# Kernel tuning notes

Hardware: AMD Instinct MI355X
Metric: run time of the kernel (lower is better)

Reference implementation:

```python
import jax, jax.numpy as jnp
import numpy as np

B, N, C, H, AD, HID = 2, 1024, 768, 12, 8, 3072
SCALE = (C // H) ** -0.5


def setup_inputs() -> dict:
    key = jax.random.key(0)
    ks = jax.random.split(key, 32)
    inp = {}
    for i in range(5):
        inp[f"x{i}"] = jax.random.normal(ks[i], (B, N, C), jnp.float32)
    def w(i, shape, s=0.02):
        return jax.random.normal(ks[i], shape, jnp.float32) * s
    inp.update({
        "ln1_g": jnp.ones((C,), jnp.float32), "ln1_b": jnp.zeros((C,), jnp.float32),
        "ln2_g": jnp.ones((C,), jnp.float32), "ln2_b": jnp.zeros((C,), jnp.float32),
        "qkv_w": w(5, (C, 3 * C)), "qkv_b": jnp.zeros((3 * C,), jnp.float32),
        "proj_w": w(6, (C, C)), "proj_b": jnp.zeros((C,), jnp.float32),
        "fc1_w": w(7, (C, HID)), "fc1_b": jnp.zeros((HID,), jnp.float32),
        "fc2_w": w(8, (HID, C)), "fc2_b": jnp.zeros((C,), jnp.float32),
        "at_dw": w(9, (C, AD)), "at_db": jnp.zeros((AD,), jnp.float32),
        "at_mw": w(10, (AD, AD)), "at_mb": jnp.zeros((AD,), jnp.float32),
        "at_uw": w(11, (AD, C)), "at_ub": jnp.zeros((C,), jnp.float32),
        "a2_dw": w(12, (C, AD)), "a2_db": jnp.zeros((AD,), jnp.float32),
        "a2_mw": w(13, (AD, AD)), "a2_mb": jnp.zeros((AD,), jnp.float32),
        "a2_uw": w(14, (AD, C)), "a2_ub": jnp.zeros((C,), jnp.float32),
    })
    return inp


def _ln(x, g, b, eps=1e-5):
    mu = x.mean(-1, keepdims=True)
    xc = x - mu
    var = (xc * xc).mean(-1, keepdims=True)
    return xc * jax.lax.rsqrt(var + eps) * g + b


def _adapter(x, dw, db, mw, mb, uw, ub):
    h = x @ dw + db          # bottleneck down [., AD]
    h = h @ mw + mb          # mid
    return h @ uw + ub       # up back to C


def _attn(x, qkv_w, qkv_b, proj_w, proj_b):
    # x: [S, B, N, C] (streams folded in leading axis)
    s, b, n, c = x.shape
    qkv = (x @ qkv_w + qkv_b).reshape(s, b, n, 3, H, c // H)
    q, k, v = jnp.moveaxis(qkv, 3, 0)            # each [S,B,N,H,D]
    scores = jnp.einsum('sbnhd,sbmhd->sbhnm', q * SCALE, k)  # fp32; clamp is a no-op
    p = jax.nn.softmax(scores, axis=-1)
    o = jnp.einsum('sbhnm,sbmhd->sbnhd', p, v).reshape(s, b, n, c)
    return o @ proj_w + proj_b


def reference(x0, x1, x2, x3, x4,
              ln1_g, ln1_b, ln2_g, ln2_b,
              qkv_w, qkv_b, proj_w, proj_b,
              fc1_w, fc1_b, fc2_w, fc2_b,
              at_dw, at_db, at_mw, at_mb, at_uw, at_ub,
              a2_dw, a2_db, a2_mw, a2_mb, a2_uw, a2_ub):
    xs = jnp.stack([x0, x1, x2, x3, x4])          # [5,B,N,C]
    n1 = _ln(xs, ln1_g, ln1_b)
    a1 = _adapter(n1, at_dw, at_db, at_mw, at_mb, at_uw, at_ub)
    ao = _attn(n1, qkv_w, qkv_b, proj_w, proj_b)
    # cross-stream residuals: x01=a1[0], x12=a1[1], ..., x10=a1[1], x21=a1[2], ...
    y0 = xs[0] + ao[0] + a1[1]
    y1 = xs[1] + ao[1] + a1[0] + a1[2]
    y2 = xs[2] + ao[2] + a1[1] + a1[3]
    y3 = xs[3] + ao[3] + a1[2] + a1[4]
    y4 = xs[4] + ao[4] + a1[3]
    ys = jnp.stack([y0, y1, y2, y3, y4])
    a2 = _adapter(_ln(ys, ln1_g, ln1_b), a2_dw, a2_db, a2_mw, a2_mb, a2_uw, a2_ub)
    h = _ln(ys, ln2_g, ln2_b) @ fc1_w + fc1_b
    m = jax.nn.gelu(h, approximate=False) @ fc2_w + fc2_b
    z0 = ys[0] + m[0] + a2[1]
    z1 = ys[1] + m[1] + a2[0] + a2[2]
    z2 = ys[2] + m[2] + a2[1] + a2[3]
    z3 = ys[3] + m[3] + a2[2] + a2[4]
    z4 = ys[4] + m[4] + a2[3]
    return jnp.stack([z0, z1, z2, z3, z4])        # [5,B,N,C]
```

## Files before the change

kernel.cpp:

```cpp
#include <hip/hip_runtime.h>
#include <math.h>

typedef __bf16 bf16;
typedef __attribute__((ext_vector_type(8))) __bf16 bf16x8;
typedef __attribute__((ext_vector_type(4))) __bf16 bf16x4;
typedef __attribute__((ext_vector_type(4))) float f32x4;
typedef __attribute__((ext_vector_type(16))) float f32x16;

#define TOK   10240
#define CD    768
#define NQKV  2304
#define NHID  3072
#define SEQ   1024
#define NH    12

__device__ __forceinline__ f32x4 mfma16(bf16x8 a, bf16x8 b, f32x4 c) {
  return __builtin_amdgcn_mfma_f32_16x16x32_bf16(a, b, c, 0, 0, 0);
}
__device__ __forceinline__ f32x16 mfma32(bf16x8 a, bf16x8 b, f32x16 c) {
  return __builtin_amdgcn_mfma_f32_32x32x16_bf16(a, b, c, 0, 0, 0);
}

__device__ __forceinline__ void gload16(const void* g, void* l) {
  __builtin_amdgcn_global_load_lds(
      (const __attribute__((address_space(1))) void*)g,
      (__attribute__((address_space(3))) void*)l, 16, 0, 0);
}

__device__ __forceinline__ unsigned pack2(bf16 a, bf16 b) {
  union { unsigned short u[2]; unsigned v; } x;
  x.u[0] = __builtin_bit_cast(unsigned short, a);
  x.u[1] = __builtin_bit_cast(unsigned short, b);
  return x.v;
}

__device__ __forceinline__ float fast_gelu(float v) {
  float u = 0.7978845608f * (v + 0.044715f * v * v * v);
  float e = __expf(fminf(2.f * u, 30.f));
  return 0.5f * v * (1.f + (e - 1.f) / (e + 1.f));
}

__global__ __launch_bounds__(256) void transpose_to_bf16(
    const float* __restrict__ in, bf16* __restrict__ out, int K, int N) {
  __shared__ float tile[32][33];
  const int bn = blockIdx.x * 32, bk = blockIdx.y * 32;
  const int r = threadIdx.x >> 5, c = threadIdx.x & 31;
#pragma unroll
  for (int i = 0; i < 4; ++i)
    tile[r + 8 * i][c] = in[(size_t)(bk + r + 8 * i) * N + bn + c];
  __syncthreads();
#pragma unroll
  for (int i = 0; i < 4; ++i)
    out[(size_t)(bn + r + 8 * i) * K + bk + c] = (bf16)tile[c][r + 8 * i];
}

__global__ __launch_bounds__(256) void ln5_kernel(
    const float* __restrict__ x0, const float* __restrict__ x1,
    const float* __restrict__ x2, const float* __restrict__ x3,
    const float* __restrict__ x4, const float* __restrict__ g,
    const float* __restrict__ b, bf16* __restrict__ out) {
  const int w = threadIdx.x >> 6, lane = threadIdx.x & 63;
  const int row = blockIdx.x * 4 + w;
  const int s = row >> 11, rem = row & 2047;
  const float* xp;
  switch (s) {
    case 0: xp = x0; break; case 1: xp = x1; break; case 2: xp = x2; break;
    case 3: xp = x3; break; default: xp = x4; break;
  }
  const f32x4* xr = (const f32x4*)(xp + (size_t)rem * CD);
  f32x4 v[3];
#pragma unroll
  for (int i = 0; i < 3; ++i) v[i] = xr[lane + 64 * i];
  float sum = 0.f;
#pragma unroll
  for (int i = 0; i < 3; ++i)
#pragma unroll
    for (int j = 0; j < 4; ++j) sum += v[i][j];
#pragma unroll
  for (int m = 32; m >= 1; m >>= 1) sum += __shfl_xor(sum, m);
  const float mu = sum * (1.f / 768.f);
  float vs = 0.f;
#pragma unroll
  for (int i = 0; i < 3; ++i)
#pragma unroll
    for (int j = 0; j < 4; ++j) { float d = v[i][j] - mu; vs += d * d; }
#pragma unroll
  for (int m = 32; m >= 1; m >>= 1) vs += __shfl_xor(vs, m);
  const float rstd = rsqrtf(vs * (1.f / 768.f) + 1e-5f);
  const f32x4* gp = (const f32x4*)g;
  const f32x4* bp = (const f32x4*)b;
  bf16* orow = out + (size_t)row * CD;
#pragma unroll
  for (int i = 0; i < 3; ++i) {
    const int c4 = lane + 64 * i;
    f32x4 gg = gp[c4], bb = bp[c4];
    bf16x4 o;
#pragma unroll
    for (int j = 0; j < 4; ++j)
      o[j] = (bf16)((v[i][j] - mu) * rstd * gg[j] + bb[j]);
    *(bf16x4*)(orow + c4 * 4) = o;
  }
}

__global__ __launch_bounds__(256) void fuse_res_ln(
    const float* __restrict__ x0, const float* __restrict__ x1,
    const float* __restrict__ x2, const float* __restrict__ x3,
    const float* __restrict__ x4, const float* __restrict__ add,
    const float* __restrict__ a, float* __restrict__ ys,
    const float* __restrict__ g1, const float* __restrict__ b1,
    const float* __restrict__ g2, const float* __restrict__ b2,
    bf16* __restrict__ o1, bf16* __restrict__ o2) {
  const int w = threadIdx.x >> 6, lane = threadIdx.x & 63;
  const int row = blockIdx.x * 4 + w;
  const int s = row >> 11, rem = row & 2047;
  const float* xp;
  switch (s) {
    case 0: xp = x0; break; case 1: xp = x1; break; case 2: xp = x2; break;
    case 3: xp = x3; break; default: xp = x4; break;
  }
  const f32x4* xr = (const f32x4*)(xp + (size_t)rem * CD);
  const f32x4* ar = (const f32x4*)(add + (size_t)row * CD);
  const f32x4* am = (const f32x4*)(a + (size_t)(row - 2048) * CD);
  const f32x4* ap = (const f32x4*)(a + (size_t)(row + 2048) * CD);
  f32x4 v[3];
#pragma unroll
  for (int i = 0; i < 3; ++i) {
    const int c4 = lane + 64 * i;
    f32x4 t = xr[c4] + ar[c4];
    if (s > 0) t += am[c4];
    if (s < 4) t += ap[c4];
    v[i] = t;
  }
  f32x4* yr = (f32x4*)(ys + (size_t)row * CD);
#pragma unroll
  for (int i = 0; i < 3; ++i) yr[lane + 64 * i] = v[i];

  float sum = 0.f;
#pragma unroll
  for (int i = 0; i < 3; ++i)
#pragma unroll
    for (int j = 0; j < 4; ++j) sum += v[i][j];
#pragma unroll
  for (int m = 32; m >= 1; m >>= 1) sum += __shfl_xor(sum, m);
  const float mu = sum * (1.f / 768.f);
  float vs = 0.f;
#pragma unroll
  for (int i = 0; i < 3; ++i)
#pragma unroll
    for (int j = 0; j < 4; ++j) { float d = v[i][j] - mu; vs += d * d; }
#pragma unroll
  for (int m = 32; m >= 1; m >>= 1) vs += __shfl_xor(vs, m);
  const float rstd = rsqrtf(vs * (1.f / 768.f) + 1e-5f);
  bf16* r1 = o1 + (size_t)row * CD;
  bf16* r2 = o2 + (size_t)row * CD;
#pragma unroll
  for (int i = 0; i < 3; ++i) {
    const int c4 = lane + 64 * i;
    f32x4 gg1 = ((const f32x4*)g1)[c4], bb1 = ((const f32x4*)b1)[c4];
    f32x4 gg2 = ((const f32x4*)g2)[c4], bb2 = ((const f32x4*)b2)[c4];
    bf16x4 oa, ob;
#pragma unroll
    for (int j = 0; j < 4; ++j) {
      float n = (v[i][j] - mu) * rstd;
      oa[j] = (bf16)(n * gg1[j] + bb1[j]);
      ob[j] = (bf16)(n * gg2[j] + bb2[j]);
    }
    *(bf16x4*)(r1 + c4 * 4) = oa;
    *(bf16x4*)(r2 + c4 * 4) = ob;
  }
}

#define GBAR() __builtin_amdgcn_s_barrier()

#define LOADA(MH, BUF)                                                      \
  _Pragma("unroll") for (int m_ = 0; m_ < 4; ++m_) {                        \
    af[m_][0] =                                                             \
        *(const bf16x8*)&As[BUF][((MH)*128 + arow + m_ * 16) * 64 + ach0];  \
    af[m_][1] =                                                             \
        *(const bf16x8*)&As[BUF][((MH)*128 + arow + m_ * 16) * 64 + ach1];  \
  }

#define LOADB(DST, NH, BUF)                                                 \
  _Pragma("unroll") for (int n_ = 0; n_ < 2; ++n_) {                        \
    DST[n_][0] =                                                            \
        *(const bf16x8*)&Bs[BUF][(brow + (NH)*32 + n_ * 16) * 64 + ach0];   \
    DST[n_][1] =                                                            \
        *(const bf16x8*)&Bs[BUF][(brow + (NH)*32 + n_ * 16) * 64 + ach1];   \
  }

#define MFMA_PH(MH, NH, BF)                                                 \
  __builtin_amdgcn_s_setprio(1);                                            \
  _Pragma("unroll") for (int m_ = 0; m_ < 4; ++m_)                          \
  _Pragma("unroll") for (int n_ = 0; n_ < 2; ++n_) {                        \
    acc[(MH)*4 + m_][(NH)*2 + n_] =                                         \
        mfma16(af[m_][0], BF[n_][0], acc[(MH)*4 + m_][(NH)*2 + n_]);        \
    acc[(MH)*4 + m_][(NH)*2 + n_] =                                         \
        mfma16(af[m_][1], BF[n_][1], acc[(MH)*4 + m_][(NH)*2 + n_]);        \
  }                                                                         \
  __builtin_amdgcn_s_setprio(0);

template <int EPI>
__global__ __launch_bounds__(512, 2) void gemm256(
    const bf16* __restrict__ A, const bf16* __restrict__ Bt,
    const float* __restrict__ bias, void* __restrict__ Cout, int N, int K,
    int nbn) {
  __shared__ bf16 As[2][16384];
  __shared__ bf16 Bs[2][16384];
  const int t = threadIdx.x, lane = t & 63, w = t >> 6;
  const int wm = w >> 2, wn = w & 3;

  const int chunkg = gridDim.x >> 3;
  const int wg = (blockIdx.x & 7) * chunkg + (blockIdx.x >> 3);
  const int bm = wg / nbn, bn = wg % nbn;

  f32x4 acc[8][4] = {};

  const int srow = t >> 3;
  const int scol = ((t & 7) ^ (srow & 7)) << 3;
  const bf16* Ab = A + (size_t)(bm * 256 + srow) * K + scol;
  const bf16* Bb = Bt + (size_t)(bn * 256 + srow) * K + scol;
  const size_t r64 = (size_t)64 * K;

  auto stage_a = [&](int buf, int h, int kt) {
    const bf16* g = Ab + (size_t)h * 128 * K + (size_t)kt * 64;
    gload16(g, &As[buf][h * 8192 + w * 512]);
    gload16(g + r64, &As[buf][h * 8192 + 4096 + w * 512]);
  };
  auto stage_b = [&](int buf, int h, int kt) {
    const bf16* g = Bb + (size_t)h * 128 * K + (size_t)kt * 64;
    gload16(g, &Bs[buf][h * 8192 + w * 512]);
    gload16(g + r64, &Bs[buf][h * 8192 + 4096 + w * 512]);
  };

  const int arow = wm * 64 + (lane & 15);
  const int brow = wn * 64 + (lane & 15);
  const int ach0 = (((lane >> 4) + 0) ^ (lane & 7)) << 3;
  const int ach1 = (((lane >> 4) + 4) ^ (lane & 7)) << 3;

  stage_a(0, 0, 0); stage_b(0, 0, 0); stage_b(0, 1, 0); stage_a(0, 1, 0);
  stage_a(1, 0, 1); stage_b(1, 0, 1);
  asm volatile("s_waitcnt vmcnt(4)" ::: "memory");
  GBAR();

  const int NT = K >> 6, NI = NT >> 1;
  bf16x8 af[4][2], bf0[2][2], bf1[2][2];

  for (int j = 0; j < NI; ++j) {
    const int tA = 2 * j, tB = 2 * j + 1;
    const bool notlast = (j + 1 < NI);

    LOADA(0, 0);
    LOADB(bf0, 0, 0);
    stage_b(1, 1, tB);
    GBAR();
    MFMA_PH(0, 0, bf0);
    GBAR();
    LOADB(bf1, 1, 0);
    stage_a(1, 1, tB);
    GBAR();
    MFMA_PH(0, 1, bf1);
    GBAR();
    LOADA(1, 0);
    if (notlast) stage_a(0, 0, tA + 2);
    GBAR();
    MFMA_PH(1, 0, bf0);
    GBAR();
    if (notlast) {
      stage_b(0, 0, tA + 2);
      asm volatile("s_waitcnt vmcnt(4)" ::: "memory");
    } else {
      asm volatile("s_waitcnt vmcnt(0)" ::: "memory");
    }
    GBAR();
    MFMA_PH(1, 1, bf1);
    GBAR();

    LOADA(0, 1);
    LOADB(bf0, 0, 1);
    if (notlast) stage_b(0, 1, tA + 2);
    GBAR();
    MFMA_PH(0, 0, bf0);
    GBAR();
    LOADB(bf1, 1, 1);
    if (notlast) stage_a(0, 1, tA + 2);
    GBAR();
    MFMA_PH(0, 1, bf1);
    GBAR();
    LOADA(1, 1);
    if (notlast) stage_a(1, 0, tB + 2);
    GBAR();
    MFMA_PH(1, 0, bf0);
    GBAR();
    if (notlast) {
      stage_b(1, 0, tB + 2);
      asm volatile("s_waitcnt vmcnt(4)" ::: "memory");
    }
    GBAR();
    MFMA_PH(1, 1, bf1);
    GBAR();
  }

#pragma unroll
  for (int am = 0; am < 8; ++am) {
    const int grow0 =
        bm * 256 + (am >> 2) * 128 + wm * 64 + (am & 3) * 16 + (lane >> 4) * 4;
#pragma unroll
    for (int an = 0; an < 4; ++an) {
      const int gcol = bn * 256 + wn * 64 + an * 16 + (lane & 15);
      const float bv = bias[gcol];
#pragma unroll
      for (int r = 0; r < 4; ++r) {
        float v = acc[am][an][r] + bv;
        if (EPI == 2) v = fast_gelu(v);
        const size_t idx = (size_t)(grow0 + r) * N + gcol;
        if (EPI == 0) ((float*)Cout)[idx] = v;
        else ((bf16*)Cout)[idx] = (bf16)v;
      }
    }
  }
}

__global__ __launch_bounds__(256, 3) void attn_v2(
    const bf16* __restrict__ qkv, bf16* __restrict__ obuf) {
  __shared__ bf16 Ks[2][4096];
  __shared__ bf16 Vt[2][4096];
  const int t = threadIdx.x, lane = t & 63, w = t >> 6;
  const int g = lane >> 5, q32 = lane & 31, rq7 = q32 & 7;

  const int xcd = blockIdx.x & 7, slot = blockIdx.x >> 3;
  const int work = xcd * 120 + slot;
  const int sbh = work >> 3, qt = work & 7;
  const int sb = sbh / NH, h = sbh % NH;
  const size_t tokbase = (size_t)sb * SEQ;
  const int qoff = h * 64, koff = CD + h * 64, voff = 2 * CD + h * 64;

  const int qrow = qt * 128 + w * 32 + q32;
  bf16x8 qf[4];
  {
    const bf16* qp = qkv + (tokbase + qrow) * NQKV + qoff + g * 8;
#pragma unroll
    for (int kd = 0; kd < 4; ++kd) {
      bf16x8 v = *(const bf16x8*)(qp + kd * 16);
#pragma unroll
      for (int j = 0; j < 8; ++j) v[j] = (bf16)((float)v[j] * 0.125f);
      qf[kd] = v;
    }
  }

  const int skv1 = t >> 3, sc1 = (t & 7) ^ (skv1 & 7);
  const int skv2 = (t + 256) >> 3, sc2 = (t & 7) ^ (skv2 & 7);
  const int vkv0 = 2 * (t & 31);
  const int vd0 = 8 * (t >> 5);
  const int c0 = (vkv0 & 51) | ((vkv0 & 4) << 1) | ((vkv0 & 8) >> 1);
  const int vchunk = c0 >> 3, vsub = c0 & 7;
  const bf16* kbase = qkv + tokbase * NQKV + koff;
  const bf16* vbase = qkv + tokbase * NQKV + voff;

  {
    const bf16* kb0 = kbase;
    gload16(kb0 + (size_t)skv1 * NQKV + sc1 * 8, &Ks[0][w * 512]);
    gload16(kb0 + (size_t)skv2 * NQKV + sc2 * 8, &Ks[0][2048 + w * 512]);
    const bf16* vp = vbase + (size_t)vkv0 * NQKV + vd0;
    bf16x8 r0 = *(const bf16x8*)vp;
    bf16x8 r1 = *(const bf16x8*)(vp + NQKV);
#pragma unroll
    for (int j = 0; j < 8; ++j) {
      const int d = vd0 + j;
      *(unsigned*)&Vt[0][d * 64 + ((vchunk ^ j) << 3) + vsub] =
          pack2(r0[j], r1[j]);
    }
  }
  __syncthreads();

  float m_run = -1e30f, l_run = 0.f;
  f32x16 oT0 = {}, oT1 = {};
  int cur = 0;

  for (int kt = 0; kt < 16; ++kt) {
    bf16x8 nv0, nv1;
    if (kt < 15) {
      const bf16* vp = vbase + (size_t)((kt + 1) * 64 + vkv0) * NQKV + vd0;
      nv0 = *(const bf16x8*)vp;
      nv1 = *(const bf16x8*)(vp + NQKV);
      const bf16* kb0 = kbase + (size_t)(kt + 1) * 64 * NQKV;
      gload16(kb0 + (size_t)skv1 * NQKV + sc1 * 8, &Ks[cur ^ 1][w * 512]);
      gload16(kb0 + (size_t)skv2 * NQKV + sc2 * 8,
              &Ks[cur ^ 1][2048 + w * 512]);
    }

    f32x16 sT0 = {}, sT1 = {};
#pragma unroll
    for (int kd = 0; kd < 4; ++kd) {
      bf16x8 kf0 =
          *(const bf16x8*)&Ks[cur][q32 * 64 + (((2 * kd + g) ^ rq7) << 3)];
      bf16x8 kf1 = *(const bf16x8*)&Ks[cur][(32 + q32) * 64 +
                                            (((2 * kd + g) ^ rq7) << 3)];
      sT0 = mfma32(kf0, qf[kd], sT0);
      sT1 = mfma32(kf1, qf[kd], sT1);
    }

    float mt = sT0[0];
#pragma unroll
    for (int r = 1; r < 16; ++r) mt = fmaxf(mt, sT0[r]);
#pragma unroll
    for (int r = 0; r < 16; ++r) mt = fmaxf(mt, sT1[r]);
    mt = fmaxf(mt, __shfl_xor(mt, 32));
    const float mnew = fmaxf(m_run, mt);
    const float alpha = __expf(m_run - mnew);
    m_run = mnew;
    float rs = 0.f;
#pragma unroll
    for (int r = 0; r < 16; ++r) {
      sT0[r] = __expf(sT0[r] - mnew);
      rs += sT0[r];
    }
#pragma unroll
    for (int r = 0; r < 16; ++r) {
      sT1[r] = __expf(sT1[r] - mnew);
      rs += sT1[r];
    }
    rs += __shfl_xor(rs, 32);
    l_run = l_run * alpha + rs;
#pragma unroll
    for (int r = 0; r < 16; ++r) { oT0[r] *= alpha; oT1[r] *= alpha; }

    bf16x8 pa[4];
#pragma unroll
    for (int hh = 0; hh < 2; ++hh)
#pragma unroll
      for (int j = 0; j < 8; ++j) {
        pa[hh][j] = (bf16)sT0[8 * hh + j];
        pa[2 + hh][j] = (bf16)sT1[8 * hh + j];
      }

#pragma unroll
    for (int ks = 0; ks < 4; ++ks) {
      bf16x8 vf0 =
          *(const bf16x8*)&Vt[cur][q32 * 64 + (((2 * ks + g) ^ rq7) << 3)];
      bf16x8 vf1 = *(const bf16x8*)&Vt[cur][(32 + q32) * 64 +
                                            (((2 * ks + g) ^ rq7) << 3)];
      oT0 = mfma32(vf0, pa[ks], oT0);
      oT1 = mfma32(vf1, pa[ks], oT1);
    }

    if (kt < 15) {
#pragma unroll
      for (int j = 0; j < 8; ++j) {
        const int d = vd0 + j;
        *(unsigned*)&Vt[cur ^ 1][d * 64 + ((vchunk ^ j) << 3) + vsub] =
            pack2(nv0[j], nv1[j]);
      }
    }
    __syncthreads();
    cur ^= 1;
  }

  const float rl = 1.f / l_run;
  bf16* orow = obuf + (tokbase + qrow) * CD + h * 64;
#pragma unroll
  for (int m = 0; m < 4; ++m) {
    bf16x4 o0, o1;
#pragma unroll
    for (int r = 0; r < 4; ++r) {
      o0[r] = (bf16)(oT0[4 * m + r] * rl);
      o1[r] = (bf16)(oT1[4 * m + r] * rl);
    }
    *(bf16x4*)(orow + 8 * m + 4 * g) = o0;
    *(bf16x4*)(orow + 32 + 8 * m + 4 * g) = o1;
  }
}

__global__ __launch_bounds__(256) void adapter_kernel(
    const bf16* __restrict__ X, const float* __restrict__ dw,
    const float* __restrict__ db, const float* __restrict__ mw,
    const float* __restrict__ mb, const float* __restrict__ uw,
    const float* __restrict__ ub, float* __restrict__ out) {
  const int tok = blockIdx.x * 4 + (threadIdx.x >> 6);
  const int lane = threadIdx.x & 63;
  const bf16* xr = X + (size_t)tok * CD;
  float xv[12];
#pragma unroll
  for (int i = 0; i < 12; ++i) xv[i] = (float)xr[lane + 64 * i];
  float h1[8] = {0, 0, 0, 0, 0, 0, 0, 0};
#pragma unroll
  for (int i = 0; i < 12; ++i) {
    const f32x4* dr = (const f32x4*)(dw + (size_t)(lane + 64 * i) * 8);
    f32x4 d0 = dr[0], d1 = dr[1];
#pragma unroll
    for (int j = 0; j < 4; ++j) {
      h1[j] += xv[i] * d0[j];
      h1[4 + j] += xv[i] * d1[j];
    }
  }
#pragma unroll
  for (int m = 1; m < 64; m <<= 1)
#pragma unroll
    for (int j = 0; j < 8; ++j) h1[j] += __shfl_xor(h1[j], m);
#pragma unroll
  for (int j = 0; j < 8; ++j) h1[j] += db[j];
  float h2[8];
#pragma unroll
  for (int k = 0; k < 8; ++k) {
    float v = mb[k];
#pragma unroll
    for (int j = 0; j < 8; ++j) v += h1[j] * mw[j * 8 + k];
    h2[k] = v;
  }
#pragma unroll
  for (int i = 0; i < 12; ++i) {
    const int c = lane + 64 * i;
    float v = ub[c];
#pragma unroll
    for (int k = 0; k < 8; ++k) v += h2[k] * uw[k * CD + c];
    out[(size_t)tok * CD + c] = v;
  }
}

__global__ __launch_bounds__(256) void cross_residual(
    const float* __restrict__ p0, const float* __restrict__ p1,
    const float* __restrict__ p2, const float* __restrict__ p3,
    const float* __restrict__ p4, const float* __restrict__ add,
    const float* __restrict__ a, float* __restrict__ out) {
  const int s = blockIdx.y;
  const size_t i = (size_t)blockIdx.x * 256 + threadIdx.x;
  const size_t spitch = (size_t)2048 * 768 / 4;
  const size_t sb = (size_t)s * spitch;
  const float* p;
  switch (s) {
    case 0: p = p0; break; case 1: p = p1; break; case 2: p = p2; break;
    case 3: p = p3; break; default: p = p4; break;
  }
  f32x4 v = ((const f32x4*)p)[i];
  v += ((const f32x4*)add)[sb + i];
  if (s > 0) v += ((const f32x4*)a)[sb - spitch + i];
  if (s < 4) v += ((const f32x4*)a)[sb + spitch + i];
  ((f32x4*)out)[sb + i] = v;
}

#define OFF_WTQKV  ((size_t)0)
#define OFF_WTPROJ ((size_t)3538944)
#define OFF_WTFC1  ((size_t)4718592)
#define OFF_WTFC2  ((size_t)9437184)
#define OFF_N1     ((size_t)14155776)
#define OFF_BIG    ((size_t)29884416)
#define OFF_OBUF   ((size_t)77070336)
#define OFF_AOM    ((size_t)92798976)
#define OFF_A12    ((size_t)124256256)
#define OFF_YS     ((size_t)155713536)
#define OFF_L2Y    ((size_t)187170816)

extern "C" void kernel_launch(void* const* d_in, const int* in_sizes, int n_in,
                              void* d_out, int out_size, void* d_ws,
                              size_t ws_size, hipStream_t stream) {
  const float* x0 = (const float*)d_in[0];
  const float* x1 = (const float*)d_in[1];
  const float* x2 = (const float*)d_in[2];
  const float* x3 = (const float*)d_in[3];
  const float* x4 = (const float*)d_in[4];
  const float* ln1_g = (const float*)d_in[5];
  const float* ln1_b = (const float*)d_in[6];
  const float* ln2_g = (const float*)d_in[7];
  const float* ln2_b = (const float*)d_in[8];
  const float* qkv_w = (const float*)d_in[9];
  const float* qkv_b = (const float*)d_in[10];
  const float* proj_w = (const float*)d_in[11];
  const float* proj_b = (const float*)d_in[12];
  const float* fc1_w = (const float*)d_in[13];
  const float* fc1_b = (const float*)d_in[14];
  const float* fc2_w = (const float*)d_in[15];
  const float* fc2_b = (const float*)d_in[16];
  const float* at_dw = (const float*)d_in[17];
  const float* at_db = (const float*)d_in[18];
  const float* at_mw = (const float*)d_in[19];
  const float* at_mb = (const float*)d_in[20];
  const float* at_uw = (const float*)d_in[21];
  const float* at_ub = (const float*)d_in[22];
  const float* a2_dw = (const float*)d_in[23];
  const float* a2_db = (const float*)d_in[24];
  const float* a2_mw = (const float*)d_in[25];
  const float* a2_mb = (const float*)d_in[26];
  const float* a2_uw = (const float*)d_in[27];
  const float* a2_ub = (const float*)d_in[28];

  char* ws = (char*)d_ws;
  bf16* wt_qkv = (bf16*)(ws + OFF_WTQKV);
  bf16* wt_proj = (bf16*)(ws + OFF_WTPROJ);
  bf16* wt_fc1 = (bf16*)(ws + OFF_WTFC1);
  bf16* wt_fc2 = (bf16*)(ws + OFF_WTFC2);
  bf16* n1 = (bf16*)(ws + OFF_N1);
  bf16* qkvb = (bf16*)(ws + OFF_BIG);
  bf16* obuf = (bf16*)(ws + OFF_OBUF);
  float* aom = (float*)(ws + OFF_AOM);
  float* a12 = (float*)(ws + OFF_A12);
  float* ysb = (float*)(ws + OFF_YS);
  bf16* l2y = (bf16*)(ws + OFF_L2Y);

  const dim3 b256(256);
  const dim3 b512(512);

  transpose_to_bf16<<<dim3(72, 24), b256, 0, stream>>>(qkv_w, wt_qkv, 768, 2304);
  transpose_to_bf16<<<dim3(24, 24), b256, 0, stream>>>(proj_w, wt_proj, 768, 768);
  transpose_to_bf16<<<dim3(96, 24), b256, 0, stream>>>(fc1_w, wt_fc1, 768, 3072);
  transpose_to_bf16<<<dim3(24, 96), b256, 0, stream>>>(fc2_w, wt_fc2, 3072, 768);

  ln5_kernel<<<2560, b256, 0, stream>>>(x0, x1, x2, x3, x4, ln1_g, ln1_b, n1);

  gemm256<1><<<360, b512, 0, stream>>>(n1, wt_qkv, qkv_b, qkvb, NQKV, 768, 9);

  adapter_kernel<<<2560, b256, 0, stream>>>(n1, at_dw, at_db, at_mw, at_mb,
                                            at_uw, at_ub, a12);

  attn_v2<<<960, b256, 0, stream>>>(qkvb, obuf);

  gemm256<0><<<120, b512, 0, stream>>>(obuf, wt_proj, proj_b, aom, CD, 768, 3);

  fuse_res_ln<<<2560, b256, 0, stream>>>(x0, x1, x2, x3, x4, aom, a12, ysb,
                                         ln1_g, ln1_b, ln2_g, ln2_b, n1, l2y);

  adapter_kernel<<<2560, b256, 0, stream>>>(n1, a2_dw, a2_db, a2_mw, a2_mb,
                                            a2_uw, a2_ub, a12);

  gemm256<2><<<480, b512, 0, stream>>>(l2y, wt_fc1, fc1_b, qkvb, NHID, 768, 12);

  gemm256<0><<<120, b512, 0, stream>>>(qkvb, wt_fc2, fc2_b, aom, CD, NHID, 3);

  const size_t sp = (size_t)2048 * 768;
  cross_residual<<<dim3(1536, 5), b256, 0, stream>>>(
      ysb, ysb + sp, ysb + 2 * sp, ysb + 3 * sp, ysb + 4 * sp, aom, a12,
      (float*)d_out);
}
```

Baseline: 416.2 us.

## Split-K the fc2 GEMM and store adapter and partial outputs in bf16

Adds split-K support to the GEMM (k-partition index, leading dimension, per-partition output stride). The fc2 GEMM now runs as two K halves over 240 blocks, so the 120-block launch no longer underfills the GPU. Each half writes a bf16 partial buffer, and the final cross-residual kernel sums the two. Adapter outputs are also stored as bf16, cutting memory traffic in fuse_res_ln and cross_residual, at some precision cost from bf16 rounding of the partials and adapter values.

```diff
diff --git a/kernel.cpp b/kernel.cpp
--- a/kernel.cpp
+++ b/kernel.cpp
@@ -32,6 +32,14 @@
   x.u[0] = __builtin_bit_cast(unsigned short, a);
   x.u[1] = __builtin_bit_cast(unsigned short, b);
   return x.v;
+}
+
+__device__ __forceinline__ f32x4 b4tof(const bf16* p) {
+  bf16x4 v = *(const bf16x4*)p;
+  f32x4 r;
+#pragma unroll
+  for (int j = 0; j < 4; ++j) r[j] = (float)v[j];
+  return r;
 }
 
 __device__ __forceinline__ float fast_gelu(float v) {
@@ -106,7 +114,7 @@
     const float* __restrict__ x0, const float* __restrict__ x1,
     const float* __restrict__ x2, const float* __restrict__ x3,
     const float* __restrict__ x4, const float* __restrict__ add,
-    const float* __restrict__ a, float* __restrict__ ys,
+    const bf16* __restrict__ a, float* __restrict__ ys,
     const float* __restrict__ g1, const float* __restrict__ b1,
     const float* __restrict__ g2, const float* __restrict__ b2,
     bf16* __restrict__ o1, bf16* __restrict__ o2) {
@@ -120,15 +128,15 @@
   }
   const f32x4* xr = (const f32x4*)(xp + (size_t)rem * CD);
   const f32x4* ar = (const f32x4*)(add + (size_t)row * CD);
-  const f32x4* am = (const f32x4*)(a + (size_t)(row - 2048) * CD);
-  const f32x4* ap = (const f32x4*)(a + (size_t)(row + 2048) * CD);
+  const bf16* am = a + (size_t)(row - 2048) * CD;
+  const bf16* ap = a + (size_t)(row + 2048) * CD;
   f32x4 v[3];
 #pragma unroll
   for (int i = 0; i < 3; ++i) {
     const int c4 = lane + 64 * i;
     f32x4 t = xr[c4] + ar[c4];
-    if (s > 0) t += am[c4];
-    if (s < 4) t += ap[c4];
+    if (s > 0) t += b4tof(am + c4 * 4);
+    if (s < 4) t += b4tof(ap + c4 * 4);
     v[i] = t;
   }
   f32x4* yr = (f32x4*)(ys + (size_t)row * CD);
@@ -202,8 +210,8 @@
 template <int EPI>
 __global__ __launch_bounds__(512, 2) void gemm256(
     const bf16* __restrict__ A, const bf16* __restrict__ Bt,
-    const float* __restrict__ bias, void* __restrict__ Cout, int N, int K,
-    int nbn) {
+    const float* __restrict__ bias, void* __restrict__ Cout, int N, int Klen,
+    int ldk, int nbn, int bpk, size_t kpstride) {
   __shared__ bf16 As[2][16384];
   __shared__ bf16 Bs[2][16384];
   const int t = threadIdx.x, lane = t & 63, w = t >> 6;
@@ -211,23 +219,25 @@
 
   const int chunkg = gridDim.x >> 3;
   const int wg = (blockIdx.x & 7) * chunkg + (blockIdx.x >> 3);
-  const int bm = wg / nbn, bn = wg % nbn;
+  const int kp = wg / bpk, rem = wg % bpk;
+  const int bm = rem / nbn, bn = rem % nbn;
 
   f32x4 acc[8][4] = {};
 
   const int srow = t >> 3;
   const int scol = ((t & 7) ^ (srow & 7)) << 3;
-  const bf16* Ab = A + (size_t)(bm * 256 + srow) * K + scol;
-  const bf16* Bb = Bt + (size_t)(bn * 256 + srow) * K + scol;
-  const size_t r64 = (size_t)64 * K;
+  const size_t koff = (size_t)kp * Klen;
+  const bf16* Ab = A + (size_t)(bm * 256 + srow) * ldk + koff + scol;
+  const bf16* Bb = Bt + (size_t)(bn * 256 + srow) * ldk + koff + scol;
+  const size_t r64 = (size_t)64 * ldk;
 
   auto stage_a = [&](int buf, int h, int kt) {
-    const bf16* g = Ab + (size_t)h * 128 * K + (size_t)kt * 64;
+    const bf16* g = Ab + (size_t)h * 128 * ldk + (size_t)kt * 64;
     gload16(g, &As[buf][h * 8192 + w * 512]);
     gload16(g + r64, &As[buf][h * 8192 + 4096 + w * 512]);
   };
   auto stage_b = [&](int buf, int h, int kt) {
-    const bf16* g = Bb + (size_t)h * 128 * K + (size_t)kt * 64;
+    const bf16* g = Bb + (size_t)h * 128 * ldk + (size_t)kt * 64;
     gload16(g, &Bs[buf][h * 8192 + w * 512]);
     gload16(g + r64, &Bs[buf][h * 8192 + 4096 + w * 512]);
   };
@@ -242,7 +252,7 @@
   asm volatile("s_waitcnt vmcnt(4)" ::: "memory");
   GBAR();
 
-  const int NT = K >> 6, NI = NT >> 1;
+  const int NT = Klen >> 6, NI = NT >> 1;
   bf16x8 af[4][2], bf0[2][2], bf1[2][2];
 
   for (int j = 0; j < NI; ++j) {
@@ -307,12 +317,12 @@
 #pragma unroll
     for (int an = 0; an < 4; ++an) {
       const int gcol = bn * 256 + wn * 64 + an * 16 + (lane & 15);
-      const float bv = bias[gcol];
+      const float bv = (kp == 0) ? bias[gcol] : 0.f;
 #pragma unroll
       for (int r = 0; r < 4; ++r) {
         float v = acc[am][an][r] + bv;
         if (EPI == 2) v = fast_gelu(v);
-        const size_t idx = (size_t)(grow0 + r) * N + gcol;
+        const size_t idx = (size_t)(grow0 + r) * N + gcol + kp * kpstride;
         if (EPI == 0) ((float*)Cout)[idx] = v;
         else ((bf16*)Cout)[idx] = (bf16)v;
       }
@@ -474,7 +484,7 @@
     const bf16* __restrict__ X, const float* __restrict__ dw,
     const float* __restrict__ db, const float* __restrict__ mw,
     const float* __restrict__ mb, const float* __restrict__ uw,
-    const float* __restrict__ ub, float* __restrict__ out) {
+    const float* __restrict__ ub, bf16* __restrict__ out) {
   const int tok = blockIdx.x * 4 + (threadIdx.x >> 6);
   const int lane = threadIdx.x & 63;
   const bf16* xr = X + (size_t)tok * CD;
@@ -512,28 +522,23 @@
     float v = ub[c];
 #pragma unroll
     for (int k = 0; k < 8; ++k) v += h2[k] * uw[k * CD + c];
-    out[(size_t)tok * CD + c] = v;
+    out[(size_t)tok * CD + c] = (bf16)v;
   }
 }
 
 __global__ __launch_bounds__(256) void cross_residual(
-    const float* __restrict__ p0, const float* __restrict__ p1,
-    const float* __restrict__ p2, const float* __restrict__ p3,
-    const float* __restrict__ p4, const float* __restrict__ add,
-    const float* __restrict__ a, float* __restrict__ out) {
+    const float* __restrict__ ys, const bf16* __restrict__ m01,
+    const bf16* __restrict__ a, float* __restrict__ out) {
   const int s = blockIdx.y;
   const size_t i = (size_t)blockIdx.x * 256 + threadIdx.x;
   const size_t spitch = (size_t)2048 * 768 / 4;
   const size_t sb = (size_t)s * spitch;
-  const float* p;
-  switch (s) {
-    case 0: p = p0; break; case 1: p = p1; break; case 2: p = p2; break;
-    case 3: p = p3; break; default: p = p4; break;
-  }
-  f32x4 v = ((const f32x4*)p)[i];
-  v += ((const f32x4*)add)[sb + i];
-  if (s > 0) v += ((const f32x4*)a)[sb - spitch + i];
-  if (s < 4) v += ((const f32x4*)a)[sb + spitch + i];
+  const size_t mstride = (size_t)TOK * CD / 4;
+  f32x4 v = ((const f32x4*)ys)[sb + i];
+  v += b4tof(m01 + (sb + i) * 4);
+  v += b4tof(m01 + (mstride + sb + i) * 4);
+  if (s > 0) v += b4tof(a + (sb - spitch + i) * 4);
+  if (s < 4) v += b4tof(a + (sb + spitch + i) * 4);
   ((f32x4*)out)[sb + i] = v;
 }
 
@@ -590,8 +595,9 @@
   bf16* n1 = (bf16*)(ws + OFF_N1);
   bf16* qkvb = (bf16*)(ws + OFF_BIG);
   bf16* obuf = (bf16*)(ws + OFF_OBUF);
-  float* aom = (float*)(ws + OFF_AOM);
-  float* a12 = (float*)(ws + OFF_A12);
+  float* aof = (float*)(ws + OFF_AOM);
+  bf16* mbuf = (bf16*)(ws + OFF_AOM);
+  bf16* a12 = (bf16*)(ws + OFF_A12);
   float* ysb = (float*)(ws + OFF_YS);
   bf16* l2y = (bf16*)(ws + OFF_L2Y);
 
@@ -605,27 +611,29 @@
 
   ln5_kernel<<<2560, b256, 0, stream>>>(x0, x1, x2, x3, x4, ln1_g, ln1_b, n1);
 
-  gemm256<1><<<360, b512, 0, stream>>>(n1, wt_qkv, qkv_b, qkvb, NQKV, 768, 9);
+  gemm256<1><<<360, b512, 0, stream>>>(n1, wt_qkv, qkv_b, qkvb, NQKV, 768, 768,
+                                       9, 360, 0);
 
   adapter_kernel<<<2560, b256, 0, stream>>>(n1, at_dw, at_db, at_mw, at_mb,
                                             at_uw, at_ub, a12);
 
   attn_v2<<<960, b256, 0, stream>>>(qkvb, obuf);
 
-  gemm256<0><<<120, b512, 0, stream>>>(obuf, wt_proj, proj_b, aom, CD, 768, 3);
-
-  fuse_res_ln<<<2560, b256, 0, stream>>>(x0, x1, x2, x3, x4, aom, a12, ysb,
+  gemm256<0><<<120, b512, 0, stream>>>(obuf, wt_proj, proj_b, aof, CD, 768,
+                                       768, 3, 120, 0);
+
+  fuse_res_ln<<<2560, b256, 0, stream>>>(x0, x1, x2, x3, x4, aof, a12, ysb,
                                          ln1_g, ln1_b, ln2_g, ln2_b, n1, l2y);
 
   adapter_kernel<<<2560, b256, 0, stream>>>(n1, a2_dw, a2_db, a2_mw, a2_mb,
                                             a2_uw, a2_ub, a12);
 
-  gemm256<2><<<480, b512, 0, stream>>>(l2y, wt_fc1, fc1_b, qkvb, NHID, 768, 12);
-
-  gemm256<0><<<120, b512, 0, stream>>>(qkvb, wt_fc2, fc2_b, aom, CD, NHID, 3);
-
-  const size_t sp = (size_t)2048 * 768;
-  cross_residual<<<dim3(1536, 5), b256, 0, stream>>>(
-      ysb, ysb + sp, ysb + 2 * sp, ysb + 3 * sp, ysb + 4 * sp, aom, a12,
-      (float*)d_out);
-}
+  gemm256<2><<<480, b512, 0, stream>>>(l2y, wt_fc1, fc1_b, qkvb, NHID, 768,
+                                       768, 12, 480, 0);
+
+  gemm256<1><<<240, b512, 0, stream>>>(qkvb, wt_fc2, fc2_b, mbuf, CD, 1536,
+                                       3072, 3, 120, (size_t)TOK * CD);
+
+  cross_residual<<<dim3(1536, 5), b256, 0, stream>>>(ysb, mbuf, a12,
+                                                     (float*)d_out);
+}
```

New measurement: 382.9 us. -8.0%, faster.
